# Kernel tuning notes

Measured on AMD Instinct MI355X. Metric: run time of the kernel, lower is better.

Reference implementation:

```python
import jax, jax.numpy as jnp
import numpy as np

B, L, D = 4, 2048, 1024
NUM_HEADS = 1
HEAD_DIM = D // NUM_HEADS  # 1024


def setup_inputs() -> dict:
    key = jax.random.key(0)
    ks = jax.random.split(key, 12)
    s = 1.0 / np.sqrt(D)
    return {
        "query": jax.random.normal(ks[0], (B, L, D), jnp.float32),
        "key": jax.random.normal(ks[1], (B, L, D), jnp.float32),
        "value": jax.random.normal(ks[2], (B, L, D), jnp.float32),
        "mask": jax.random.randint(ks[3], (B, 1, L, L), 0, 2, jnp.int32),
        "Wq": jax.random.uniform(ks[4], (D, D * NUM_HEADS), jnp.float32, -s, s),
        "bq": jnp.zeros((D * NUM_HEADS,), jnp.float32),
        "Wk": jax.random.uniform(ks[5], (D, D * NUM_HEADS), jnp.float32, -s, s),
        "bk": jnp.zeros((D * NUM_HEADS,), jnp.float32),
        "Wv": jax.random.uniform(ks[6], (D, D * NUM_HEADS), jnp.float32, -s, s),
        "bv": jnp.zeros((D * NUM_HEADS,), jnp.float32),
        "Wo": jax.random.uniform(ks[7], (D * NUM_HEADS, D), jnp.float32, -s, s),
        "bo": jnp.zeros((D,), jnp.float32),
    }


def reference(query, key, value, mask, Wq, bq, Wk, bk, Wv, bv, Wo, bo):
    b, lq = query.shape[0], query.shape[1]
    lk = key.shape[1]
    # project and split heads: (B, L, H, Dh) -> (B, H, L, Dh)
    Q = (query @ Wq + bq).reshape(b, lq, NUM_HEADS, HEAD_DIM).transpose(0, 2, 1, 3)
    K = (key @ Wk + bk).reshape(b, lk, NUM_HEADS, HEAD_DIM).transpose(0, 2, 1, 3)
    V = (value @ Wv + bv).reshape(b, lk, NUM_HEADS, HEAD_DIM).transpose(0, 2, 1, 3)
    scale = 1.0 / jnp.sqrt(jnp.float32(HEAD_DIM))
    scores = jnp.einsum("bhqd,bhkd->bhqk", Q, K) * scale  # (B,H,Lq,Lk)
    scores = jnp.where(mask == 0, jnp.float32(-1e20), scores)
    attn = jax.nn.softmax(scores, axis=-1)
    out = jnp.einsum("bhqk,bhkd->bhqd", attn, V)  # (B,H,Lq,Dh)
    out = out.transpose(0, 2, 1, 3).reshape(b, lq, NUM_HEADS * HEAD_DIM)
    return out @ Wo + bo
```

## Files before the change

### kernel.cpp

```cpp
#include <hip/hip_runtime.h>

#define B_ 4
#define L_ 2048
#define D_ 1024
#define M_FLAT (B_*L_)

typedef unsigned short bf16_t;
typedef __attribute__((ext_vector_type(8))) short bf16x8;
typedef __attribute__((ext_vector_type(4))) float f32x4;

__device__ __forceinline__ bf16_t f2bf(float f) {
  union { float f; unsigned int u; } c; c.f = f;
  unsigned int u = c.u;
  unsigned int r = (u + 0x7fffu + ((u >> 16) & 1u)) >> 16;
  return (bf16_t)r;
}
__device__ __forceinline__ float bf2f(bf16_t h) {
  union { unsigned int u; float f; } c; c.u = ((unsigned int)h) << 16;
  return c.f;
}

__device__ __forceinline__ void gload_lds16(const bf16_t* g, bf16_t* l) {
  __builtin_amdgcn_global_load_lds(
      (const __attribute__((address_space(1))) unsigned int*)g,
      (__attribute__((address_space(3))) unsigned int*)l, 16, 0, 0);
}

#define BARRIER() do { asm volatile("" ::: "memory"); \
                       __builtin_amdgcn_s_barrier();  \
                       asm volatile("" ::: "memory"); } while (0)

__global__ __launch_bounds__(256) void cvt_bf16(const float* __restrict__ in,
                                                bf16_t* __restrict__ out) {
  size_t i = (size_t)blockIdx.x * 256 + threadIdx.x;
  const float4* p = (const float4*)in + i * 2;
  float4 a = p[0], b = p[1];
  union { bf16_t h[8]; uint4 u; } r;
  r.h[0] = f2bf(a.x); r.h[1] = f2bf(a.y); r.h[2] = f2bf(a.z); r.h[3] = f2bf(a.w);
  r.h[4] = f2bf(b.x); r.h[5] = f2bf(b.y); r.h[6] = f2bf(b.z); r.h[7] = f2bf(b.w);
  ((uint4*)out)[i] = r.u;
}

__global__ __launch_bounds__(256) void transpose_cvt(const float* __restrict__ Wsrc,
                                                     bf16_t* __restrict__ Wt) {
  __shared__ float t[32][33];
  int c0 = blockIdx.x * 32, r0 = blockIdx.y * 32;
  int tx = threadIdx.x, ty = threadIdx.y;
#pragma unroll
  for (int i = 0; i < 4; i++)
    t[ty + i * 8][tx] = Wsrc[(size_t)(r0 + ty + i * 8) * D_ + c0 + tx];
  __syncthreads();
#pragma unroll
  for (int i = 0; i < 4; i++)
    Wt[(size_t)(c0 + ty + i * 8) * D_ + r0 + tx] = f2bf(t[tx][ty + i * 8]);
}

__global__ __launch_bounds__(256) void transpose_bf16(const bf16_t* __restrict__ in,
                                                      bf16_t* __restrict__ out,
                                                      int R, int C, long strIn, long strOut) {
  __shared__ bf16_t t[32][33];
  int c0 = blockIdx.x * 32, r0 = blockIdx.y * 32;
  int tx = threadIdx.x, ty = threadIdx.y;
  const bf16_t* ip = in + (size_t)blockIdx.z * strIn;
  bf16_t* op = out + (size_t)blockIdx.z * strOut;
#pragma unroll
  for (int i = 0; i < 4; i++)
    t[ty + i * 8][tx] = ip[(size_t)(r0 + ty + i * 8) * C + c0 + tx];
  __syncthreads();
#pragma unroll
  for (int i = 0; i < 4; i++)
    op[(size_t)(c0 + ty + i * 8) * R + r0 + tx] = t[tx][ty + i * 8];
}

__global__ __launch_bounds__(256) void c2_kernel(const float* __restrict__ bv,
                                                 const float* __restrict__ Wo,
                                                 float* __restrict__ c2) {
  int j = blockIdx.x * 256 + threadIdx.x;
  float s = 0.f;
  for (int k = 0; k < D_; k++) s += bv[k] * Wo[(size_t)k * D_ + j];
  c2[j] = s;
}

__global__ __launch_bounds__(256) void softmax_row(bf16_t* __restrict__ S,
                                                   const int* __restrict__ mask,
                                                   float* __restrict__ rs) {
  int row = blockIdx.x;
  int tid = threadIdx.x;
  uint4* p = (uint4*)(S + (size_t)row * L_);
  const int4* mp = (const int4*)(mask + (size_t)row * L_) + tid * 2;
  int4 m0 = mp[0], m1 = mp[1];
  union { uint4 u; bf16_t h[8]; } v;
  v.u = p[tid];
  int mk[8] = {m0.x, m0.y, m0.z, m0.w, m1.x, m1.y, m1.z, m1.w};
  float sum = 0.f;
#pragma unroll
  for (int j = 0; j < 8; j++) {
    float e = (mk[j] != 0) ? __expf(bf2f(v.h[j])) : 0.0f;
    bf16_t eb = f2bf(e);
    v.h[j] = eb;
    sum += bf2f(eb);
  }
  p[tid] = v.u;
#pragma unroll
  for (int off = 32; off; off >>= 1) sum += __shfl_down(sum, off, 64);
  __shared__ float wsum[4];
  if ((tid & 63) == 0) wsum[tid >> 6] = sum;
  __syncthreads();
  if (tid == 0) rs[row] = fmaxf(wsum[0] + wsum[1] + wsum[2] + wsum[3], 1e-30f);
}

#define MODE_PROJ 0
#define MODE_BF16 1
#define MODE_FIN  2

template <int BM, int MODE>
__global__ __launch_bounds__(512, 2)
void g8(const bf16_t* __restrict__ Abase, int lda, long strA,
        const bf16_t* __restrict__ Bbase, int ldb, long strB,
        void* __restrict__ outp, long strO, int ldo,
        const float* __restrict__ x0, const float* __restrict__ x1,
        const float* __restrict__ x2, int K) {
  constexpr int WROWS = BM / 2;
  constexpr int QAF   = WROWS / 32;
  constexpr int MFR   = WROWS / 16;
  constexpr int AL    = BM / 128;
  constexpr int BL    = 2;
  constexpr int AHB   = WROWS * 128;
  constexpr int BUFB  = (BM + 256) * 128;
  extern __shared__ __align__(16) char smem[];

  const int tid = threadIdx.x, lane = tid & 63, w = tid >> 6;
  const int wm = w >> 2, wn = w & 3;
  const int fr = lane & 15, fs = lane >> 4;
  const int z = blockIdx.z;

  int gx = gridDim.x, nxy = gx * gridDim.y;
  int lin = blockIdx.y * gx + blockIdx.x;
  if ((nxy & 7) == 0) { int q = nxy >> 3; lin = (lin & 7) * q + (lin >> 3); }
  const int mbase = (lin / gx) * BM, nbase = (lin % gx) * 256;

  const bf16_t* A  = Abase + (size_t)z * strA;
  const bf16_t* Bt = Bbase + (size_t)z * strB;

  int offA[2][2], offB[2][2];
#pragma unroll
  for (int h = 0; h < 2; h++)
#pragma unroll
    for (int i = 0; i < 2; i++) {
      int c = i * 512 + tid, row = c >> 3;
      int sg = (c & 7) ^ (row & 7);
      if (i < AL) offA[h][i] = (mbase + h * WROWS + row) * lda + sg * 8;
      offB[h][i] = (nbase + h * 128 + row) * ldb + sg * 8;
    }

  const int swz0 = (fs ^ (fr & 7)) * 16;
  const int swz1 = ((4 + fs) ^ (fr & 7)) * 16;

  bf16x8 af[QAF][2], bfv[2][2][2];
  f32x4 acc[MFR][4] = {};

#define STAGE_A(h, kt, bsel) do {                                             \
    char* hb_ = smem + (bsel) * BUFB + (h) * AHB;                             \
    _Pragma("unroll")                                                         \
    for (int i_ = 0; i_ < AL; ++i_)                                           \
      gload_lds16(A + offA[h][i_] + (kt) * 64,                                \
                  (bf16_t*)(hb_ + (i_ * 512 + tid) * 16));                    \
  } while (0)
#define STAGE_B(h, kt, bsel) do {                                             \
    char* hb_ = smem + (bsel) * BUFB + BM * 128 + (h) * 16384;                \
    _Pragma("unroll")                                                         \
    for (int i_ = 0; i_ < BL; ++i_)                                           \
      gload_lds16(Bt + offB[h][i_] + (kt) * 64,                               \
                  (bf16_t*)(hb_ + (i_ * 512 + tid) * 16));                    \
  } while (0)
#define LOAD_A(bsel, mh) do {                                                 \
    const char* ab_ = smem + (bsel) * BUFB + (wm * WROWS) * 128;              \
    _Pragma("unroll")                                                         \
    for (int i_ = 0; i_ < QAF; ++i_) {                                        \
      int rb_ = ((mh) * (WROWS / 2) + i_ * 16 + fr) * 128;                    \
      af[i_][0] = *(const bf16x8*)(ab_ + rb_ + swz0);                         \
      af[i_][1] = *(const bf16x8*)(ab_ + rb_ + swz1);                         \
    }                                                                         \
  } while (0)
#define LOAD_B(bsel, nh) do {                                                 \
    const char* bb_ = smem + (bsel) * BUFB + BM * 128 + (wn * 64) * 128;      \
    _Pragma("unroll")                                                         \
    for (int j_ = 0; j_ < 2; ++j_) {                                          \
      int rb_ = ((nh) * 32 + j_ * 16 + fr) * 128;                             \
      bfv[nh][j_][0] = *(const bf16x8*)(bb_ + rb_ + swz0);                    \
      bfv[nh][j_][1] = *(const bf16x8*)(bb_ + rb_ + swz1);                    \
    }                                                                         \
  } while (0)
#define MFMA_Q(mh, nh) do {                                                   \
    __builtin_amdgcn_s_setprio(1);                                            \
    _Pragma("unroll")                                                         \
    for (int i_ = 0; i_ < QAF; ++i_)                                          \
    _Pragma("unroll")                                                         \
    for (int j_ = 0; j_ < 2; ++j_) {                                          \
      acc[(mh)*QAF + i_][(nh)*2 + j_] = __builtin_amdgcn_mfma_f32_16x16x32_bf16( \
          af[i_][0], bfv[nh][j_][0], acc[(mh)*QAF + i_][(nh)*2 + j_], 0, 0, 0);  \
      acc[(mh)*QAF + i_][(nh)*2 + j_] = __builtin_amdgcn_mfma_f32_16x16x32_bf16( \
          af[i_][1], bfv[nh][j_][1], acc[(mh)*QAF + i_][(nh)*2 + j_], 0, 0, 0);  \
    }                                                                         \
    __builtin_amdgcn_s_setprio(0);                                            \
  } while (0)
#define LGKM0() do { asm volatile("s_waitcnt lgkmcnt(0)" ::: "memory");       \
                     __builtin_amdgcn_sched_barrier(0); } while (0)

  const int NK = K >> 6, NI = NK >> 1;

  STAGE_B(0, 0, 0); STAGE_B(1, 0, 0); STAGE_A(0, 0, 0); STAGE_A(1, 0, 0);
  STAGE_B(0, 1, 1); STAGE_A(0, 1, 1);
  if constexpr (AL == 2) asm volatile("s_waitcnt vmcnt(4)" ::: "memory");
  else                   asm volatile("s_waitcnt vmcnt(3)" ::: "memory");
  BARRIER();

  for (int it = 0; it < NI; ++it) {
    const int t1 = 2 * it + 1;
    const int ta = (2 * it + 2 < NK) ? 2 * it + 2 : NK - 1;
    const int tb = (2 * it + 3 < NK) ? 2 * it + 3 : NK - 1;
    LOAD_A(0, 0); LOAD_B(0, 0);
    STAGE_B(1, t1, 1);
    BARRIER(); LGKM0(); MFMA_Q(0, 0); BARRIER();
    LOAD_B(0, 1);
    STAGE_A(1, t1, 1);
    BARRIER(); LGKM0(); MFMA_Q(0, 1); BARRIER();
    LOAD_A(0, 1);
    STAGE_B(0, ta, 0);
    BARRIER(); LGKM0(); MFMA_Q(1, 1); BARRIER();
    STAGE_B(1, ta, 0);
    asm volatile("s_waitcnt vmcnt(4)" ::: "memory");
    BARRIER(); MFMA_Q(1, 0); BARRIER();
    LOAD_A(1, 0); LOAD_B(1, 0);
    STAGE_A(0, ta, 0);
    BARRIER(); LGKM0(); MFMA_Q(0, 0); BARRIER();
    LOAD_B(1, 1);
    STAGE_A(1, ta, 0);
    BARRIER(); LGKM0(); MFMA_Q(0, 1); BARRIER();
    LOAD_A(1, 1);
    STAGE_B(0, tb, 1);
    BARRIER(); LGKM0(); MFMA_Q(1, 1); BARRIER();
    STAGE_A(0, tb, 1);
    if constexpr (AL == 2) asm volatile("s_waitcnt vmcnt(4)" ::: "memory");
    else                   asm volatile("s_waitcnt vmcnt(3)" ::: "memory");
    BARRIER(); MFMA_Q(1, 0); BARRIER();
  }
  asm volatile("s_waitcnt vmcnt(0)" ::: "memory");

  const int r0 = mbase + wm * WROWS;
  const int c0 = nbase + wn * 64;

  if constexpr (MODE == MODE_PROJ) {
    const float* bias = (z == 0) ? x0 : (z == 1) ? x1 : x2;
    const float scale = (z == 0) ? 0.03125f : 1.0f;
    bf16_t* o = (bf16_t*)outp + (size_t)z * strO;
#pragma unroll
    for (int nf = 0; nf < 4; ++nf) {
      int c = c0 + nf * 16 + fr;
      float bv = bias[c];
#pragma unroll
      for (int mf = 0; mf < MFR; ++mf) {
        int rr = r0 + mf * 16 + fs * 4;
#pragma unroll
        for (int jj = 0; jj < 4; ++jj)
          o[(size_t)(rr + jj) * ldo + c] = f2bf((acc[mf][nf][jj] + bv) * scale);
      }
    }
  } else if constexpr (MODE == MODE_BF16) {
    bf16_t* o = (bf16_t*)outp + (size_t)z * strO;
#pragma unroll
    for (int nf = 0; nf < 4; ++nf) {
      int c = c0 + nf * 16 + fr;
#pragma unroll
      for (int mf = 0; mf < MFR; ++mf) {
        int rr = r0 + mf * 16 + fs * 4;
#pragma unroll
        for (int jj = 0; jj < 4; ++jj)
          o[(size_t)(rr + jj) * ldo + c] = f2bf(acc[mf][nf][jj]);
      }
    }
  } else {
    float* o = (float*)outp + (size_t)z * strO;
    const float* rs = x0 + (size_t)z * L_;
#pragma unroll
    for (int mf = 0; mf < MFR; ++mf) {
#pragma unroll
      for (int jj = 0; jj < 4; ++jj) {
        int r = r0 + mf * 16 + fs * 4 + jj;
        float inv = 1.0f / rs[r];
#pragma unroll
        for (int nf = 0; nf < 4; ++nf) {
          int c = c0 + nf * 16 + fr;
          o[(size_t)r * ldo + c] = acc[mf][nf][jj] * inv + x1[c];
        }
      }
    }
  }
#undef STAGE_A
#undef STAGE_B
#undef LOAD_A
#undef LOAD_B
#undef MFMA_Q
#undef LGKM0
}

extern "C" void kernel_launch(void* const* d_in, const int* in_sizes, int n_in,
                              void* d_out, int out_size, void* d_ws, size_t ws_size,
                              hipStream_t stream) {
  const float* query = (const float*)d_in[0];
  const float* keyi  = (const float*)d_in[1];
  const float* value = (const float*)d_in[2];
  const int*   mask  = (const int*)d_in[3];
  const float* Wq = (const float*)d_in[4];
  const float* bq = (const float*)d_in[5];
  const float* Wk = (const float*)d_in[6];
  const float* bk = (const float*)d_in[7];
  const float* Wv = (const float*)d_in[8];
  const float* bv = (const float*)d_in[9];
  const float* Wo = (const float*)d_in[10];
  const float* bo = (const float*)d_in[11];

  bf16_t* ws = (bf16_t*)d_ws;
  const size_t NE = (size_t)M_FLAT * D_;
  const size_t WE = (size_t)D_ * D_;
  bf16_t* XQ   = ws;
  bf16_t* XK   = ws + NE;
  bf16_t* XV   = ws + 2 * NE;
  bf16_t* WQT  = ws + 3 * NE;
  bf16_t* WKT  = WQT + WE;
  bf16_t* W2T  = WKT + WE;
  bf16_t* WOT  = W2T + WE;
  bf16_t* WVb  = WOT + WE;
  bf16_t* Qb   = WVb + WE;
  bf16_t* Kb   = Qb + NE;
  bf16_t* VW   = Kb + NE;
  bf16_t* W2tmp= VW + NE;
  float*  rsump= (float*)(W2tmp + WE);
  float*  c2p  = rsump + (size_t)B_ * L_;
  bf16_t* Sb   = ws;
  bf16_t* VWt  = XV;

  hipFuncSetAttribute((const void*)g8<256, MODE_PROJ>,
                      hipFuncAttributeMaxDynamicSharedMemorySize, 131072);
  hipFuncSetAttribute((const void*)g8<256, MODE_BF16>,
                      hipFuncAttributeMaxDynamicSharedMemorySize, 131072);
  hipFuncSetAttribute((const void*)g8<128, MODE_BF16>,
                      hipFuncAttributeMaxDynamicSharedMemorySize, 98304);
  hipFuncSetAttribute((const void*)g8<128, MODE_FIN>,
                      hipFuncAttributeMaxDynamicSharedMemorySize, 98304);

  cvt_bf16<<<dim3(4096), dim3(256), 0, stream>>>(query, XQ);
  cvt_bf16<<<dim3(4096), dim3(256), 0, stream>>>(keyi, XK);
  cvt_bf16<<<dim3(4096), dim3(256), 0, stream>>>(value, XV);
  cvt_bf16<<<dim3(512), dim3(256), 0, stream>>>(Wv, WVb);
  transpose_cvt<<<dim3(32, 32), dim3(32, 8), 0, stream>>>(Wq, WQT);
  transpose_cvt<<<dim3(32, 32), dim3(32, 8), 0, stream>>>(Wk, WKT);
  transpose_cvt<<<dim3(32, 32), dim3(32, 8), 0, stream>>>(Wo, WOT);
  c2_kernel<<<dim3(4), dim3(256), 0, stream>>>(bv, Wo, c2p);
  g8<128, MODE_BF16><<<dim3(4, 8, 1), 512, 98304, stream>>>(
      WVb, D_, 0, WOT, D_, 0, W2tmp, 0, D_,
      nullptr, nullptr, nullptr, D_);
  transpose_bf16<<<dim3(32, 32, 1), dim3(32, 8), 0, stream>>>(
      W2tmp, W2T, D_, D_, 0, 0);
  g8<256, MODE_PROJ><<<dim3(4, 32, 3), 512, 131072, stream>>>(
      XQ, D_, (long)NE, WQT, D_, (long)WE, Qb, (long)NE, D_,
      bq, bk, c2p, D_);
  transpose_bf16<<<dim3(32, 64, 4), dim3(32, 8), 0, stream>>>(
      VW, VWt, L_, D_, (long)L_ * D_, (long)D_ * L_);
  g8<256, MODE_BF16><<<dim3(8, 8, 4), 512, 131072, stream>>>(
      Qb, D_, (long)L_ * D_, Kb, D_, (long)L_ * D_, Sb, (long)L_ * L_, L_,
      nullptr, nullptr, nullptr, D_);
  softmax_row<<<dim3(B_ * L_), dim3(256), 0, stream>>>(Sb, mask, rsump);
  g8<128, MODE_FIN><<<dim3(4, 16, 4), 512, 98304, stream>>>(
      Sb, L_, (long)L_ * L_, VWt, L_, (long)D_ * L_, d_out, (long)L_ * D_, D_,
      rsump, bo, nullptr, L_);
}
```

Before: 263.3 us.

## Restructure GEMM prefetch schedule and stage bf16 epilogue through LDS for vector stores

Reorders the global-to-LDS staging in the main GEMM loop so both halves of the next k-tile are issued together at fixed points, with a single deeper vmcnt wait. The goal is fewer wait points and more loads in flight. Separately, the bf16 and projection epilogues now write accumulators into a swizzled LDS buffer per wave and read them back, so each lane issues 16-byte coalesced global stores instead of scattered 2-byte stores. This costs an extra barrier and LDS traffic, and it assumes the LDS region can be reused after the main loop.

```diff
diff --git a/kernel.cpp b/kernel.cpp
--- a/kernel.cpp
+++ b/kernel.cpp
@@ -206,43 +206,39 @@
   } while (0)
 #define LGKM0() do { asm volatile("s_waitcnt lgkmcnt(0)" ::: "memory");       \
                      __builtin_amdgcn_sched_barrier(0); } while (0)
+#define VMW() do {                                                            \
+    if constexpr (AL == 2) asm volatile("s_waitcnt vmcnt(8)" ::: "memory");   \
+    else                   asm volatile("s_waitcnt vmcnt(6)" ::: "memory");   \
+  } while (0)
 
   const int NK = K >> 6, NI = NK >> 1;
 
   STAGE_B(0, 0, 0); STAGE_B(1, 0, 0); STAGE_A(0, 0, 0); STAGE_A(1, 0, 0);
-  STAGE_B(0, 1, 1); STAGE_A(0, 1, 1);
-  if constexpr (AL == 2) asm volatile("s_waitcnt vmcnt(4)" ::: "memory");
-  else                   asm volatile("s_waitcnt vmcnt(3)" ::: "memory");
-  BARRIER();
+  STAGE_B(0, 1, 1); STAGE_B(1, 1, 1); STAGE_A(0, 1, 1); STAGE_A(1, 1, 1);
+  VMW(); BARRIER();
 
   for (int it = 0; it < NI; ++it) {
-    const int t1 = 2 * it + 1;
     const int ta = (2 * it + 2 < NK) ? 2 * it + 2 : NK - 1;
     const int tb = (2 * it + 3 < NK) ? 2 * it + 3 : NK - 1;
     LOAD_A(0, 0); LOAD_B(0, 0);
-    STAGE_B(1, t1, 1);
     BARRIER(); LGKM0(); MFMA_Q(0, 0); BARRIER();
     LOAD_B(0, 1);
-    STAGE_A(1, t1, 1);
     BARRIER(); LGKM0(); MFMA_Q(0, 1); BARRIER();
     LOAD_A(0, 1);
-    STAGE_B(0, ta, 0);
+    STAGE_B(0, ta, 0); STAGE_B(1, ta, 0);
     BARRIER(); LGKM0(); MFMA_Q(1, 1); BARRIER();
-    STAGE_B(1, ta, 0);
-    asm volatile("s_waitcnt vmcnt(4)" ::: "memory");
+    STAGE_A(0, ta, 0); STAGE_A(1, ta, 0);
+    VMW();
     BARRIER(); MFMA_Q(1, 0); BARRIER();
     LOAD_A(1, 0); LOAD_B(1, 0);
-    STAGE_A(0, ta, 0);
     BARRIER(); LGKM0(); MFMA_Q(0, 0); BARRIER();
     LOAD_B(1, 1);
-    STAGE_A(1, ta, 0);
     BARRIER(); LGKM0(); MFMA_Q(0, 1); BARRIER();
     LOAD_A(1, 1);
-    STAGE_B(0, tb, 1);
+    STAGE_B(0, tb, 1); STAGE_B(1, tb, 1);
     BARRIER(); LGKM0(); MFMA_Q(1, 1); BARRIER();
-    STAGE_A(0, tb, 1);
-    if constexpr (AL == 2) asm volatile("s_waitcnt vmcnt(4)" ::: "memory");
-    else                   asm volatile("s_waitcnt vmcnt(3)" ::: "memory");
+    STAGE_A(0, tb, 1); STAGE_A(1, tb, 1);
+    VMW();
     BARRIER(); MFMA_Q(1, 0); BARRIER();
   }
   asm volatile("s_waitcnt vmcnt(0)" ::: "memory");
@@ -250,34 +246,37 @@
   const int r0 = mbase + wm * WROWS;
   const int c0 = nbase + wn * 64;
 
-  if constexpr (MODE == MODE_PROJ) {
-    const float* bias = (z == 0) ? x0 : (z == 1) ? x1 : x2;
-    const float scale = (z == 0) ? 0.03125f : 1.0f;
+  if constexpr (MODE == MODE_PROJ || MODE == MODE_BF16) {
+    BARRIER();
+    char* ep = smem + w * AHB;
     bf16_t* o = (bf16_t*)outp + (size_t)z * strO;
+    const float* bias = nullptr;
+    float scale = 1.0f;
+    if constexpr (MODE == MODE_PROJ) {
+      bias = (z == 0) ? x0 : (z == 1) ? x1 : x2;
+      scale = (z == 0) ? 0.03125f : 1.0f;
+    }
 #pragma unroll
     for (int nf = 0; nf < 4; ++nf) {
-      int c = c0 + nf * 16 + fr;
-      float bv = bias[c];
-#pragma unroll
-      for (int mf = 0; mf < MFR; ++mf) {
-        int rr = r0 + mf * 16 + fs * 4;
-#pragma unroll
-        for (int jj = 0; jj < 4; ++jj)
-          o[(size_t)(rr + jj) * ldo + c] = f2bf((acc[mf][nf][jj] + bv) * scale);
-      }
-    }
-  } else if constexpr (MODE == MODE_BF16) {
-    bf16_t* o = (bf16_t*)outp + (size_t)z * strO;
-#pragma unroll
-    for (int nf = 0; nf < 4; ++nf) {
-      int c = c0 + nf * 16 + fr;
-#pragma unroll
-      for (int mf = 0; mf < MFR; ++mf) {
-        int rr = r0 + mf * 16 + fs * 4;
-#pragma unroll
-        for (int jj = 0; jj < 4; ++jj)
-          o[(size_t)(rr + jj) * ldo + c] = f2bf(acc[mf][nf][jj]);
-      }
+      float bv = 0.0f;
+      if constexpr (MODE == MODE_PROJ) bv = bias[c0 + nf * 16 + fr];
+#pragma unroll
+      for (int mf = 0; mf < MFR; ++mf)
+#pragma unroll
+        for (int jj = 0; jj < 4; ++jj) {
+          int row = mf * 16 + fs * 4 + jj;
+          int slot = (nf * 2 + (fr >> 3)) ^ ((row >> 1) & 7);
+          *(bf16_t*)(ep + row * 128 + slot * 16 + (fr & 7) * 2) =
+              f2bf((acc[mf][nf][jj] + bv) * scale);
+        }
+    }
+    const int rl = lane >> 3, sl = lane & 7;
+#pragma unroll
+    for (int i = 0; i < WROWS / 8; ++i) {
+      int row = i * 8 + rl;
+      int slot = sl ^ ((row >> 1) & 7);
+      uint4 v = *(const uint4*)(ep + row * 128 + slot * 16);
+      *(uint4*)&o[(size_t)(r0 + row) * ldo + c0 + sl * 8] = v;
     }
   } else {
     float* o = (float*)outp + (size_t)z * strO;
@@ -302,6 +301,7 @@
 #undef LOAD_B
 #undef MFMA_Q
 #undef LGKM0
+#undef VMW
 }
 
 extern "C" void kernel_launch(void* const* d_in, const int* in_sizes, int n_in,
```

After: 262.5 us. Within noise of the previous version (-0.3%).
